# Kernel tuning notes

Measured on AMD Instinct MI355X. Metric: run time of the kernel, lower is better.

Reference implementation:

```python
import jax, jax.numpy as jnp
import numpy as np

C_M, C_Z, C_H = 256, 128, 32
LN_EPS = 1e-5


def setup_inputs() -> dict:
    key = jax.random.key(0)
    ks = jax.random.split(key, 8)
    B, N_SEQ, S = 1, 128, 256
    m = jax.random.normal(ks[0], (B, N_SEQ, S, C_M), dtype=jnp.float32)
    ln_w = jnp.ones((C_M,), jnp.float32)
    ln_b = jnp.zeros((C_M,), jnp.float32)
    Wa = jax.random.normal(ks[1], (C_M, C_H), jnp.float32) / np.sqrt(C_M)
    ba = jnp.zeros((C_H,), jnp.float32)
    Wb = jax.random.normal(ks[2], (C_M, C_H), jnp.float32) / np.sqrt(C_M)
    bb = jnp.zeros((C_H,), jnp.float32)
    Wo = jax.random.normal(ks[3], (C_H * C_H, C_Z), jnp.float32) / np.sqrt(C_H * C_H)
    bo = jnp.zeros((C_Z,), jnp.float32)
    return {"m": m, "ln_w": ln_w, "ln_b": ln_b, "Wa": Wa, "ba": ba,
            "Wb": Wb, "bb": bb, "Wo": Wo, "bo": bo}


def reference(m, ln_w, ln_b, Wa, ba, Wb, bb, Wo, bo):
    B, n_seq, S, _ = m.shape
    # LayerNorm over c_m
    mu = jnp.mean(m, axis=-1, keepdims=True)
    var = jnp.var(m, axis=-1, keepdims=True)
    mn = (m - mu) * jax.lax.rsqrt(var + LN_EPS) * ln_w + ln_b
    # dual projections: [B, n_seq, S, c_hidden]
    a = mn @ Wa + ba
    b = mn @ Wb + bb
    # outer product mean contracted over MSA rows s: [B, S, S, c_h, c_h]
    outer = jnp.einsum('bsic,bsjd->bijcd', a, b) / n_seq
    outer = outer.reshape(B, S, S, C_H * C_H)
    z_update = outer @ Wo + bo  # [B, S, S, c_z]
    return z_update
```

## Files before the change

### kernel.cpp

```cpp
#include <hip/hip_runtime.h>
#include <stdint.h>

#define NS 128
#define NR 256
#define CM 256
#define CH 32
#define CZ 128

typedef __attribute__((ext_vector_type(4))) float f32x4;
typedef __attribute__((ext_vector_type(16))) float f32x16;
typedef __attribute__((ext_vector_type(8))) short bf16x8;
typedef __attribute__((ext_vector_type(4))) unsigned short u16x4;
typedef __attribute__((ext_vector_type(4))) unsigned int u32x4;

__device__ __forceinline__ unsigned short bf16rne(float x) {
    unsigned int u = __builtin_bit_cast(unsigned int, x);
    return (unsigned short)((u + 0x7FFFu + ((u >> 16) & 1u)) >> 16);
}

__device__ __forceinline__ unsigned int pack2_bf16(float lo, float hi) {
    return (unsigned int)bf16rne(lo) | ((unsigned int)bf16rne(hi) << 16);
}

__global__ __launch_bounds__(256) void k_wrepack(const float* __restrict__ Wa,
                                                 const float* __restrict__ Wb,
                                                 const float* __restrict__ Wo,
                                                 unsigned short* __restrict__ Wab_f,
                                                 unsigned short* __restrict__ Wo_f) {
    int idx = blockIdx.x * 256 + threadIdx.x;
    int l = idx & 63;
    int lo = l & 15, hi = l >> 4;
    int il = l & 31, h = l >> 5;
    if (idx < 2048) {
        int ks = (idx >> 6) & 7;
        int n = idx >> 9;
        int k = n * 16 + lo;
        bf16x8 v;
#pragma unroll
        for (int e = 0; e < 8; ++e) {
            int c = ks * 32 + hi * 8 + e;
            float wv = (k < CH) ? Wa[c * CH + k] : Wb[c * CH + (k - CH)];
            v[e] = (short)bf16rne(wv);
        }
        *reinterpret_cast<bf16x8*>(Wab_f + (size_t)idx * 8) = v;
    } else if (idx < 2048 + 16384) {
        int t = idx - 2048;
        int ks2 = (t >> 6) & 1, kt = (t >> 7) & 3, c = t >> 9;
        bf16x8 v;
#pragma unroll
        for (int e = 0; e < 8; ++e) {
            int d = ks2 * 16 + h * 8 + e;
            v[e] = (short)bf16rne(Wo[(size_t)(c * 32 + d) * CZ + kt * 32 + il]);
        }
        *reinterpret_cast<bf16x8*>(Wo_f + (size_t)t * 8) = v;
    }
}

__global__ __launch_bounds__(256) void k_lnproj(const float* __restrict__ m,
                                                const float* __restrict__ lnw,
                                                const float* __restrict__ lnb,
                                                const float* __restrict__ ba,
                                                const float* __restrict__ bb,
                                                const unsigned short* __restrict__ Wab_f,
                                                unsigned short* __restrict__ a_n,
                                                unsigned short* __restrict__ b_n) {
    __shared__ unsigned short mn_lds[64 * 256];
    const int tid = threadIdx.x, l = tid & 63, w = tid >> 6;
    const int lo = l & 15, hi = l >> 4;
    const int R0 = blockIdx.x * 64;

    float4 wv = *reinterpret_cast<const float4*>(lnw + l * 4);
    float4 bv = *reinterpret_cast<const float4*>(lnb + l * 4);

    for (int t = 0; t < 16; ++t) {
        int row = w * 16 + t;
        int gr = R0 + row;
        float4 x = *reinterpret_cast<const float4*>(m + (size_t)gr * CM + l * 4);
        float sum = x.x + x.y + x.z + x.w;
        float sq = x.x * x.x + x.y * x.y + x.z * x.z + x.w * x.w;
#pragma unroll
        for (int off = 32; off; off >>= 1) {
            sum += __shfl_xor(sum, off);
            sq  += __shfl_xor(sq, off);
        }
        float mu = sum * (1.f / CM);
        float rstd = rsqrtf(sq * (1.f / CM) - mu * mu + 1e-5f);
        u16x4 pk;
        pk[0] = bf16rne((x.x - mu) * rstd * wv.x + bv.x);
        pk[1] = bf16rne((x.y - mu) * rstd * wv.y + bv.y);
        pk[2] = bf16rne((x.z - mu) * rstd * wv.z + bv.z);
        pk[3] = bf16rne((x.w - mu) * rstd * wv.w + bv.w);
        int byte = row * 512 + l * 8;
        byte ^= (row & 7) << 4;
        *reinterpret_cast<u16x4*>(reinterpret_cast<char*>(mn_lds) + byte) = pk;
    }

    f32x4 acc[4];
#pragma unroll
    for (int n = 0; n < 4; ++n) acc[n] = (f32x4){0.f, 0.f, 0.f, 0.f};
    const int arow = w * 16 + lo;
#pragma unroll
    for (int ks = 0; ks < 8; ++ks) {
        int byte = arow * 512 + ks * 64 + hi * 16;
        byte ^= (arow & 7) << 4;
        bf16x8 afrag = *reinterpret_cast<const bf16x8*>(reinterpret_cast<const char*>(mn_lds) + byte);
#pragma unroll
        for (int n = 0; n < 4; ++n) {
            bf16x8 bfrag = *reinterpret_cast<const bf16x8*>(Wab_f + (size_t)((n * 8 + ks) * 64 + l) * 8);
            acc[n] = __builtin_amdgcn_mfma_f32_16x16x32_bf16(afrag, bfrag, acc[n], 0, 0, 0);
        }
    }
#pragma unroll
    for (int n = 0; n < 4; ++n) {
        int k = n * 16 + lo;
        float bias = (k < CH) ? ba[k] : bb[k - CH];
#pragma unroll
        for (int r = 0; r < 4; ++r) {
            int gr = R0 + w * 16 + hi * 4 + r;
            unsigned short hv = bf16rne(acc[n][r] + bias);
            if (k < CH) a_n[(size_t)gr * CH + k] = hv;
            else        b_n[(size_t)gr * CH + (k - CH)] = hv;
        }
    }
}

__global__ __launch_bounds__(256) void k_abrepack(const unsigned short* __restrict__ a_n,
                                                  const unsigned short* __restrict__ b_n,
                                                  unsigned short* __restrict__ a_f,
                                                  unsigned short* __restrict__ b_f) {
    int idx = blockIdx.x * 256 + threadIdx.x;
    int l = idx & 63, il = l & 31, h = (l >> 5) & 1;
    if (idx < 131072) {
        int ks = (idx >> 6) & 7, ib = (idx >> 9) & 7, c = idx >> 12;
        int i = ib * 32 + il;
        bf16x8 v;
#pragma unroll
        for (int e = 0; e < 8; ++e) {
            int s = ks * 16 + h * 8 + e;
            v[e] = (short)a_n[((size_t)s * NR + i) * CH + c];
        }
        *reinterpret_cast<bf16x8*>(a_f + (size_t)idx * 8) = v;
    } else {
        int t = idx - 131072;
        int ks = (t >> 6) & 7, jl = (t >> 9) & 7, jb = t >> 12;
        int j = jb * 8 + jl;
        bf16x8 v;
#pragma unroll
        for (int e = 0; e < 8; ++e) {
            int s = ks * 16 + h * 8 + e;
            v[e] = (short)b_n[((size_t)s * NR + j) * CH + il];
        }
        *reinterpret_cast<bf16x8*>(b_f + (size_t)t * 8) = v;
    }
}

__global__ __launch_bounds__(512) void k_outer(const unsigned short* __restrict__ a_f,
                                               const unsigned short* __restrict__ b_f,
                                               const unsigned short* __restrict__ Wo_f,
                                               const float* __restrict__ bo,
                                               float* __restrict__ out) {
    __shared__ unsigned short b_lds[32768];
    __shared__ unsigned short s_af[2][4096];
    __shared__ unsigned short s_wo[2][4096];
    const int tid = threadIdx.x, l = tid & 63, w = tid >> 6;
    const int il = l & 31, h = l >> 5;
    const int bi = blockIdx.x >> 5, bj = blockIdx.x & 31;

    {
        const unsigned short* src = b_f + (size_t)bj * 32768;
#pragma unroll
        for (int it = 0; it < 8; ++it) {
            int off = it * 4096 + tid * 8;
            *reinterpret_cast<bf16x8*>(b_lds + off) =
                *reinterpret_cast<const bf16x8*>(src + off);
        }
    }
    {
        const unsigned short* srcA = a_f + (size_t)bi * 4096;
        const unsigned short* srcW = Wo_f;
        *reinterpret_cast<bf16x8*>(&s_af[0][tid * 8]) =
            *reinterpret_cast<const bf16x8*>(srcA + tid * 8);
        *reinterpret_cast<bf16x8*>(&s_wo[0][tid * 8]) =
            *reinterpret_cast<const bf16x8*>(srcW + tid * 8);
    }
    __syncthreads();

    bf16x8 bfr[8];
#pragma unroll
    for (int ks = 0; ks < 8; ++ks)
        bfr[ks] = *reinterpret_cast<const bf16x8*>(b_lds + ((w * 8 + ks) * 64 + l) * 8);

    f32x16 zacc[4];
#pragma unroll
    for (int kt = 0; kt < 4; ++kt)
        zacc[kt] = (f32x16){0.f,0.f,0.f,0.f,0.f,0.f,0.f,0.f,0.f,0.f,0.f,0.f,0.f,0.f,0.f,0.f};

    for (int c = 0; c < 32; ++c) {
        const int cur = c & 1, nxt = cur ^ 1;

        bf16x8 rA, rW;
        if (c + 1 < 32) {
            rA = *reinterpret_cast<const bf16x8*>(a_f + (size_t)((c + 1) * 8 + bi) * 4096 + tid * 8);
            rW = *reinterpret_cast<const bf16x8*>(Wo_f + (size_t)(c + 1) * 4096 + tid * 8);
        }

        bf16x8 af[8];
#pragma unroll
        for (int ks = 0; ks < 8; ++ks)
            af[ks] = *reinterpret_cast<const bf16x8*>(&s_af[cur][(ks * 64 + l) * 8]);
        bf16x8 wof0[4], wof1[4];
#pragma unroll
        for (int kt = 0; kt < 4; ++kt) {
            wof0[kt] = *reinterpret_cast<const bf16x8*>(&s_wo[cur][((kt * 2 + 0) * 64 + l) * 8]);
            wof1[kt] = *reinterpret_cast<const bf16x8*>(&s_wo[cur][((kt * 2 + 1) * 64 + l) * 8]);
        }

        f32x16 o0 = (f32x16){0.f,0.f,0.f,0.f,0.f,0.f,0.f,0.f,0.f,0.f,0.f,0.f,0.f,0.f,0.f,0.f};
        f32x16 o1 = (f32x16){0.f,0.f,0.f,0.f,0.f,0.f,0.f,0.f,0.f,0.f,0.f,0.f,0.f,0.f,0.f,0.f};
#pragma unroll
        for (int ks = 0; ks < 4; ++ks) {
            o0 = __builtin_amdgcn_mfma_f32_32x32x16_bf16(bfr[ks],     af[ks],     o0, 0, 0, 0);
            o1 = __builtin_amdgcn_mfma_f32_32x32x16_bf16(bfr[ks + 4], af[ks + 4], o1, 0, 0, 0);
        }
        f32x16 o = o0 + o1;

        unsigned int u0 = pack2_bf16(o[0],  o[1]);
        unsigned int u1 = pack2_bf16(o[2],  o[3]);
        unsigned int u2 = pack2_bf16(o[4],  o[5]);
        unsigned int u3 = pack2_bf16(o[6],  o[7]);
        unsigned int u4 = pack2_bf16(o[8],  o[9]);
        unsigned int u5 = pack2_bf16(o[10], o[11]);
        unsigned int u6 = pack2_bf16(o[12], o[13]);
        unsigned int u7 = pack2_bf16(o[14], o[15]);
        unsigned int p0 = __shfl_xor(u0, 32);
        unsigned int p1 = __shfl_xor(u1, 32);
        unsigned int p2 = __shfl_xor(u2, 32);
        unsigned int p3 = __shfl_xor(u3, 32);
        unsigned int p4 = __shfl_xor(u4, 32);
        unsigned int p5 = __shfl_xor(u5, 32);
        unsigned int p6 = __shfl_xor(u6, 32);
        unsigned int p7 = __shfl_xor(u7, 32);
        u32x4 t0 = h ? (u32x4){p0, p1, u0, u1} : (u32x4){u0, u1, p0, p1};
        u32x4 t1 = h ? (u32x4){p2, p3, u2, u3} : (u32x4){u2, u3, p2, p3};
        u32x4 t2 = h ? (u32x4){p4, p5, u4, u5} : (u32x4){u4, u5, p4, p5};
        u32x4 t3 = h ? (u32x4){p6, p7, u6, u7} : (u32x4){u6, u7, p6, p7};
        u32x4 lo16 = h ? t1 : t0;
        u32x4 hi16 = h ? t3 : t2;
        bf16x8 paA = __builtin_bit_cast(bf16x8, lo16);
        bf16x8 paB = __builtin_bit_cast(bf16x8, hi16);

#pragma unroll
        for (int kt = 0; kt < 4; ++kt) {
            zacc[kt] = __builtin_amdgcn_mfma_f32_32x32x16_bf16(paA, wof0[kt], zacc[kt], 0, 0, 0);
            zacc[kt] = __builtin_amdgcn_mfma_f32_32x32x16_bf16(paB, wof1[kt], zacc[kt], 0, 0, 0);
        }

        if (c + 1 < 32) {
            *reinterpret_cast<bf16x8*>(&s_af[nxt][tid * 8]) = rA;
            *reinterpret_cast<bf16x8*>(&s_wo[nxt][tid * 8]) = rW;
        }
        __syncthreads();
    }

    const int j = bj * 8 + w;
#pragma unroll
    for (int kt = 0; kt < 4; ++kt) {
        float bok = bo[kt * 32 + il];
#pragma unroll
        for (int r = 0; r < 16; ++r) {
            int i = bi * 32 + (r & 3) + 8 * (r >> 2) + 4 * h;
            out[((size_t)i * NR + j) * CZ + kt * 32 + il] = zacc[kt][r] * (1.f / NS) + bok;
        }
    }
}

extern "C" void kernel_launch(void* const* d_in, const int* in_sizes, int n_in,
                              void* d_out, int out_size, void* d_ws, size_t ws_size,
                              hipStream_t stream) {
    const float* m   = (const float*)d_in[0];
    const float* lnw = (const float*)d_in[1];
    const float* lnb = (const float*)d_in[2];
    const float* Wa  = (const float*)d_in[3];
    const float* ba  = (const float*)d_in[4];
    const float* Wb  = (const float*)d_in[5];
    const float* bb  = (const float*)d_in[6];
    const float* Wo  = (const float*)d_in[7];
    const float* bo  = (const float*)d_in[8];
    float* out = (float*)d_out;

    unsigned short* ws    = (unsigned short*)d_ws;
    unsigned short* a_n   = ws;
    unsigned short* b_n   = ws + 1048576;
    unsigned short* a_f   = ws + 2097152;
    unsigned short* b_f   = ws + 3145728;
    unsigned short* Wab_f = ws + 4194304;
    unsigned short* Wo_f  = ws + 4210688;
    const size_t WS_NEEDED = (size_t)(4210688 + 131072) * 2;
    if (ws_size < WS_NEEDED) return;

    k_wrepack<<<72, 256, 0, stream>>>(Wa, Wb, Wo, Wab_f, Wo_f);
    k_lnproj<<<512, 256, 0, stream>>>(m, lnw, lnb, ba, bb, Wab_f, a_n, b_n);
    k_abrepack<<<1024, 256, 0, stream>>>(a_n, b_n, a_f, b_f);
    k_outer<<<256, 512, 0, stream>>>(a_f, b_f, Wo_f, bo, out);
}
```

Before: 68.79 us.

## Software-pipeline outer-product MFMAs with previous chunk's Wo projection, request 2 blocks/CU

Restructures the k_outer channel loop so the Wo projection MFMAs for chunk c-1 are issued before the outer-product MFMAs for chunk c. This lets the independent MFMA chains interleave, hiding the dependency through bf16 packing and cross-lane shuffles. A prologue and epilogue handle the first and last chunks, and the Wo fragments are carried across iterations in registers. It also adds a min-blocks-per-CU hint of 2 to launch_bounds, which may cap registers and cause spills given the larger live state.

```diff
diff --git a/kernel.cpp b/kernel.cpp
--- a/kernel.cpp
+++ b/kernel.cpp
@@ -154,11 +154,11 @@
     }
 }
 
-__global__ __launch_bounds__(512) void k_outer(const unsigned short* __restrict__ a_f,
-                                               const unsigned short* __restrict__ b_f,
-                                               const unsigned short* __restrict__ Wo_f,
-                                               const float* __restrict__ bo,
-                                               float* __restrict__ out) {
+__global__ __launch_bounds__(512, 2) void k_outer(const unsigned short* __restrict__ a_f,
+                                                  const unsigned short* __restrict__ b_f,
+                                                  const unsigned short* __restrict__ Wo_f,
+                                                  const float* __restrict__ bo,
+                                                  float* __restrict__ out) {
     __shared__ unsigned short b_lds[32768];
     __shared__ unsigned short s_af[2][4096];
     __shared__ unsigned short s_wo[2][4096];
@@ -174,15 +174,13 @@
             *reinterpret_cast<bf16x8*>(b_lds + off) =
                 *reinterpret_cast<const bf16x8*>(src + off);
         }
-    }
-    {
-        const unsigned short* srcA = a_f + (size_t)bi * 4096;
-        const unsigned short* srcW = Wo_f;
-        *reinterpret_cast<bf16x8*>(&s_af[0][tid * 8]) =
-            *reinterpret_cast<const bf16x8*>(srcA + tid * 8);
-        *reinterpret_cast<bf16x8*>(&s_wo[0][tid * 8]) =
-            *reinterpret_cast<const bf16x8*>(srcW + tid * 8);
-    }
+        bf16x8 rA0 = *reinterpret_cast<const bf16x8*>(a_f + (size_t)bi * 4096 + tid * 8);
+        bf16x8 rW0 = *reinterpret_cast<const bf16x8*>(Wo_f + tid * 8);
+        *reinterpret_cast<bf16x8*>(&s_af[0][tid * 8]) = rA0;
+        *reinterpret_cast<bf16x8*>(&s_wo[0][tid * 8]) = rW0;
+    }
+    bf16x8 rA1 = *reinterpret_cast<const bf16x8*>(a_f + (size_t)(8 + bi) * 4096 + tid * 8);
+    bf16x8 rW1 = *reinterpret_cast<const bf16x8*>(Wo_f + (size_t)4096 + tid * 8);
     __syncthreads();
 
     bf16x8 bfr[8];
@@ -195,71 +193,106 @@
     for (int kt = 0; kt < 4; ++kt)
         zacc[kt] = (f32x16){0.f,0.f,0.f,0.f,0.f,0.f,0.f,0.f,0.f,0.f,0.f,0.f,0.f,0.f,0.f,0.f};
 
-    for (int c = 0; c < 32; ++c) {
-        const int cur = c & 1, nxt = cur ^ 1;
-
-        bf16x8 rA, rW;
-        if (c + 1 < 32) {
-            rA = *reinterpret_cast<const bf16x8*>(a_f + (size_t)((c + 1) * 8 + bi) * 4096 + tid * 8);
-            rW = *reinterpret_cast<const bf16x8*>(Wo_f + (size_t)(c + 1) * 4096 + tid * 8);
-        }
-
+    bf16x8 paA, paB;
+    bf16x8 wofP[8];
+    {
         bf16x8 af[8];
 #pragma unroll
         for (int ks = 0; ks < 8; ++ks)
-            af[ks] = *reinterpret_cast<const bf16x8*>(&s_af[cur][(ks * 64 + l) * 8]);
-        bf16x8 wof0[4], wof1[4];
+            af[ks] = *reinterpret_cast<const bf16x8*>(&s_af[0][(ks * 64 + l) * 8]);
 #pragma unroll
         for (int kt = 0; kt < 4; ++kt) {
-            wof0[kt] = *reinterpret_cast<const bf16x8*>(&s_wo[cur][((kt * 2 + 0) * 64 + l) * 8]);
-            wof1[kt] = *reinterpret_cast<const bf16x8*>(&s_wo[cur][((kt * 2 + 1) * 64 + l) * 8]);
-        }
-
+            wofP[kt]     = *reinterpret_cast<const bf16x8*>(&s_wo[0][((kt * 2 + 0) * 64 + l) * 8]);
+            wofP[kt + 4] = *reinterpret_cast<const bf16x8*>(&s_wo[0][((kt * 2 + 1) * 64 + l) * 8]);
+        }
         f32x16 o0 = (f32x16){0.f,0.f,0.f,0.f,0.f,0.f,0.f,0.f,0.f,0.f,0.f,0.f,0.f,0.f,0.f,0.f};
-        f32x16 o1 = (f32x16){0.f,0.f,0.f,0.f,0.f,0.f,0.f,0.f,0.f,0.f,0.f,0.f,0.f,0.f,0.f,0.f};
+        f32x16 o1 = o0;
 #pragma unroll
         for (int ks = 0; ks < 4; ++ks) {
             o0 = __builtin_amdgcn_mfma_f32_32x32x16_bf16(bfr[ks],     af[ks],     o0, 0, 0, 0);
             o1 = __builtin_amdgcn_mfma_f32_32x32x16_bf16(bfr[ks + 4], af[ks + 4], o1, 0, 0, 0);
         }
         f32x16 o = o0 + o1;
-
-        unsigned int u0 = pack2_bf16(o[0],  o[1]);
-        unsigned int u1 = pack2_bf16(o[2],  o[3]);
-        unsigned int u2 = pack2_bf16(o[4],  o[5]);
-        unsigned int u3 = pack2_bf16(o[6],  o[7]);
-        unsigned int u4 = pack2_bf16(o[8],  o[9]);
-        unsigned int u5 = pack2_bf16(o[10], o[11]);
-        unsigned int u6 = pack2_bf16(o[12], o[13]);
-        unsigned int u7 = pack2_bf16(o[14], o[15]);
-        unsigned int p0 = __shfl_xor(u0, 32);
-        unsigned int p1 = __shfl_xor(u1, 32);
-        unsigned int p2 = __shfl_xor(u2, 32);
-        unsigned int p3 = __shfl_xor(u3, 32);
-        unsigned int p4 = __shfl_xor(u4, 32);
-        unsigned int p5 = __shfl_xor(u5, 32);
-        unsigned int p6 = __shfl_xor(u6, 32);
-        unsigned int p7 = __shfl_xor(u7, 32);
+        unsigned int u0 = pack2_bf16(o[0],  o[1]),  u1 = pack2_bf16(o[2],  o[3]);
+        unsigned int u2 = pack2_bf16(o[4],  o[5]),  u3 = pack2_bf16(o[6],  o[7]);
+        unsigned int u4 = pack2_bf16(o[8],  o[9]),  u5 = pack2_bf16(o[10], o[11]);
+        unsigned int u6 = pack2_bf16(o[12], o[13]), u7 = pack2_bf16(o[14], o[15]);
+        unsigned int p0 = __shfl_xor(u0, 32), p1 = __shfl_xor(u1, 32);
+        unsigned int p2 = __shfl_xor(u2, 32), p3 = __shfl_xor(u3, 32);
+        unsigned int p4 = __shfl_xor(u4, 32), p5 = __shfl_xor(u5, 32);
+        unsigned int p6 = __shfl_xor(u6, 32), p7 = __shfl_xor(u7, 32);
         u32x4 t0 = h ? (u32x4){p0, p1, u0, u1} : (u32x4){u0, u1, p0, p1};
         u32x4 t1 = h ? (u32x4){p2, p3, u2, u3} : (u32x4){u2, u3, p2, p3};
         u32x4 t2 = h ? (u32x4){p4, p5, u4, u5} : (u32x4){u4, u5, p4, p5};
         u32x4 t3 = h ? (u32x4){p6, p7, u6, u7} : (u32x4){u6, u7, p6, p7};
-        u32x4 lo16 = h ? t1 : t0;
-        u32x4 hi16 = h ? t3 : t2;
-        bf16x8 paA = __builtin_bit_cast(bf16x8, lo16);
-        bf16x8 paB = __builtin_bit_cast(bf16x8, hi16);
+        paA = __builtin_bit_cast(bf16x8, h ? t1 : t0);
+        paB = __builtin_bit_cast(bf16x8, h ? t3 : t2);
+        *reinterpret_cast<bf16x8*>(&s_af[1][tid * 8]) = rA1;
+        *reinterpret_cast<bf16x8*>(&s_wo[1][tid * 8]) = rW1;
+    }
+    __syncthreads();
+
+    for (int c = 1; c < 32; ++c) {
+        const int cur = c & 1, nxt = cur ^ 1;
+
+        bf16x8 rA, rW;
+        if (c < 31) {
+            rA = *reinterpret_cast<const bf16x8*>(a_f + (size_t)((c + 1) * 8 + bi) * 4096 + tid * 8);
+            rW = *reinterpret_cast<const bf16x8*>(Wo_f + (size_t)(c + 1) * 4096 + tid * 8);
+        }
+
+        bf16x8 af[8];
+#pragma unroll
+        for (int ks = 0; ks < 8; ++ks)
+            af[ks] = *reinterpret_cast<const bf16x8*>(&s_af[cur][(ks * 64 + l) * 8]);
 
 #pragma unroll
         for (int kt = 0; kt < 4; ++kt) {
-            zacc[kt] = __builtin_amdgcn_mfma_f32_32x32x16_bf16(paA, wof0[kt], zacc[kt], 0, 0, 0);
-            zacc[kt] = __builtin_amdgcn_mfma_f32_32x32x16_bf16(paB, wof1[kt], zacc[kt], 0, 0, 0);
-        }
-
-        if (c + 1 < 32) {
+            zacc[kt] = __builtin_amdgcn_mfma_f32_32x32x16_bf16(paA, wofP[kt],     zacc[kt], 0, 0, 0);
+            zacc[kt] = __builtin_amdgcn_mfma_f32_32x32x16_bf16(paB, wofP[kt + 4], zacc[kt], 0, 0, 0);
+        }
+
+        f32x16 o0 = (f32x16){0.f,0.f,0.f,0.f,0.f,0.f,0.f,0.f,0.f,0.f,0.f,0.f,0.f,0.f,0.f,0.f};
+        f32x16 o1 = o0;
+#pragma unroll
+        for (int ks = 0; ks < 4; ++ks) {
+            o0 = __builtin_amdgcn_mfma_f32_32x32x16_bf16(bfr[ks],     af[ks],     o0, 0, 0, 0);
+            o1 = __builtin_amdgcn_mfma_f32_32x32x16_bf16(bfr[ks + 4], af[ks + 4], o1, 0, 0, 0);
+        }
+        f32x16 o = o0 + o1;
+
+#pragma unroll
+        for (int kt = 0; kt < 4; ++kt) {
+            wofP[kt]     = *reinterpret_cast<const bf16x8*>(&s_wo[cur][((kt * 2 + 0) * 64 + l) * 8]);
+            wofP[kt + 4] = *reinterpret_cast<const bf16x8*>(&s_wo[cur][((kt * 2 + 1) * 64 + l) * 8]);
+        }
+
+        unsigned int u0 = pack2_bf16(o[0],  o[1]),  u1 = pack2_bf16(o[2],  o[3]);
+        unsigned int u2 = pack2_bf16(o[4],  o[5]),  u3 = pack2_bf16(o[6],  o[7]);
+        unsigned int u4 = pack2_bf16(o[8],  o[9]),  u5 = pack2_bf16(o[10], o[11]);
+        unsigned int u6 = pack2_bf16(o[12], o[13]), u7 = pack2_bf16(o[14], o[15]);
+        unsigned int p0 = __shfl_xor(u0, 32), p1 = __shfl_xor(u1, 32);
+        unsigned int p2 = __shfl_xor(u2, 32), p3 = __shfl_xor(u3, 32);
+        unsigned int p4 = __shfl_xor(u4, 32), p5 = __shfl_xor(u5, 32);
+        unsigned int p6 = __shfl_xor(u6, 32), p7 = __shfl_xor(u7, 32);
+        u32x4 t0 = h ? (u32x4){p0, p1, u0, u1} : (u32x4){u0, u1, p0, p1};
+        u32x4 t1 = h ? (u32x4){p2, p3, u2, u3} : (u32x4){u2, u3, p2, p3};
+        u32x4 t2 = h ? (u32x4){p4, p5, u4, u5} : (u32x4){u4, u5, p4, p5};
+        u32x4 t3 = h ? (u32x4){p6, p7, u6, u7} : (u32x4){u6, u7, p6, p7};
+        paA = __builtin_bit_cast(bf16x8, h ? t1 : t0);
+        paB = __builtin_bit_cast(bf16x8, h ? t3 : t2);
+
+        if (c < 31) {
             *reinterpret_cast<bf16x8*>(&s_af[nxt][tid * 8]) = rA;
             *reinterpret_cast<bf16x8*>(&s_wo[nxt][tid * 8]) = rW;
         }
         __syncthreads();
+    }
+
+#pragma unroll
+    for (int kt = 0; kt < 4; ++kt) {
+        zacc[kt] = __builtin_amdgcn_mfma_f32_32x32x16_bf16(paA, wofP[kt],     zacc[kt], 0, 0, 0);
+        zacc[kt] = __builtin_amdgcn_mfma_f32_32x32x16_bf16(paB, wofP[kt + 4], zacc[kt], 0, 0, 0);
     }
 
     const int j = bj * 8 + w;
```

After: 67.68 us. Within noise of the previous version (-1.6%).
